# Performance work log

Hardware: AMD Instinct MI355X
Metric: run time of the kernel (lower is better)

## Reference

```python
import jax, jax.numpy as jnp
import numpy as np

DIM = 256
NUM_HEADS = 8
HEAD_DIM = DIM // NUM_HEADS      # 32
KEY_DIM = HEAD_DIM // 2          # attn_ratio=0.5 -> 16
SCALE = KEY_DIM ** -0.5
H_QKV = DIM + 2 * KEY_DIM * NUM_HEADS  # 512
EPS = 1e-5


def bn(y, gamma, beta, mean, var):
    # eval-mode BatchNorm2d over channel dim of NCHW
    inv = jax.lax.rsqrt(var + EPS) * gamma
    return y * inv[None, :, None, None] + (beta - mean * inv)[None, :, None, None]


def setup_inputs() -> dict:
    key = jax.random.key(0)
    ks = jax.random.split(key, 16)
    B, C, H, W = 16, DIM, 32, 32
    x = jax.random.normal(ks[0], (B, C, H, W), dtype=jnp.float32)
    w_qkv = jax.random.normal(ks[1], (H_QKV, C), dtype=jnp.float32) * 0.05
    g_qkv = jax.random.uniform(ks[2], (H_QKV,), minval=0.5, maxval=1.5)
    b_qkv = jax.random.normal(ks[3], (H_QKV,)) * 0.1
    m_qkv = jax.random.normal(ks[4], (H_QKV,)) * 0.1
    v_qkv = jax.random.uniform(ks[5], (H_QKV,), minval=0.5, maxval=1.5)
    w_pos = jax.random.normal(ks[6], (C, 1, 3, 3), dtype=jnp.float32) * 0.1
    g_pos = jax.random.uniform(ks[7], (C,), minval=0.5, maxval=1.5)
    b_pos = jax.random.normal(ks[8], (C,)) * 0.1
    m_pos = jax.random.normal(ks[9], (C,)) * 0.1
    v_pos = jax.random.uniform(ks[10], (C,), minval=0.5, maxval=1.5)
    w_proj = jax.random.normal(ks[11], (C, C), dtype=jnp.float32) * 0.05
    g_proj = jax.random.uniform(ks[12], (C,), minval=0.5, maxval=1.5)
    b_proj = jax.random.normal(ks[13], (C,)) * 0.1
    m_proj = jax.random.normal(ks[14], (C,)) * 0.1
    v_proj = jax.random.uniform(ks[15], (C,), minval=0.5, maxval=1.5)
    return dict(x=x, w_qkv=w_qkv, g_qkv=g_qkv, b_qkv=b_qkv, m_qkv=m_qkv, v_qkv=v_qkv,
                w_pos=w_pos, g_pos=g_pos, b_pos=b_pos, m_pos=m_pos, v_pos=v_pos,
                w_proj=w_proj, g_proj=g_proj, b_proj=b_proj, m_proj=m_proj, v_proj=v_proj)


def reference(x, w_qkv, g_qkv, b_qkv, m_qkv, v_qkv,
              w_pos, g_pos, b_pos, m_pos, v_pos,
              w_proj, g_proj, b_proj, m_proj, v_proj):
    B, C, H, W = x.shape
    N = H * W
    # 1x1 conv (no bias) + BN
    qkv = bn(jnp.einsum('bchw,oc->bohw', x, w_qkv), g_qkv, b_qkv, m_qkv, v_qkv)
    qkv = qkv.reshape(B, NUM_HEADS, 2 * KEY_DIM + HEAD_DIM, N)
    q = qkv[:, :, :KEY_DIM]                 # [B, h, kd, N]
    k = qkv[:, :, KEY_DIM:2 * KEY_DIM]      # [B, h, kd, N]
    v = qkv[:, :, 2 * KEY_DIM:]             # [B, h, hd, N]
    # attention: q^T k, softmax over keys
    scores = jnp.einsum('bhkn,bhkm->bhnm', q, k) * SCALE  # [B, h, N, N]
    attn = jax.nn.softmax(scores, axis=-1)
    # v @ attn^T -> [B, h, hd, N]
    attended = jnp.einsum('bhdn,bhmn->bhdm', v, attn).reshape(B, C, H, W)
    # depthwise 3x3 positional encoding on v + BN, residual add
    v_img = v.reshape(B, C, H, W)
    pos = jax.lax.conv_general_dilated(
        v_img, w_pos, window_strides=(1, 1), padding=((1, 1), (1, 1)),
        dimension_numbers=('NCHW', 'OIHW', 'NCHW'), feature_group_count=C)
    pos = bn(pos, g_pos, b_pos, m_pos, v_pos)
    out = attended + pos
    # final 1x1 projection + BN
    out = bn(jnp.einsum('bchw,oc->bohw', out, w_proj), g_proj, b_proj, m_proj, v_proj)
    return out
```

## Files before the change

### kernel.cpp

```cpp
#include <hip/hip_runtime.h>

typedef short v8s __attribute__((ext_vector_type(8)));
typedef float v4f __attribute__((ext_vector_type(4)));
typedef unsigned short u16;

#define NPIX 1024
#define EPS 1e-5f

__device__ __forceinline__ float bf2f(u16 u){
  return __uint_as_float(((unsigned)u) << 16);
}
__device__ __forceinline__ u16 f2bf(float f){
  unsigned b = __float_as_uint(f);
  b += 0x7FFF + ((b >> 16) & 1);
  return (u16)(b >> 16);
}
__device__ __forceinline__ unsigned cvtpk(float lo, float hi){
  unsigned r;
  asm("v_cvt_pk_bf16_f32 %0, %1, %2" : "=v"(r) : "v"(lo), "v"(hi));
  return r;
}
__device__ __forceinline__ float exp2n(float x){
#if __has_builtin(__builtin_amdgcn_exp2f)
  return __builtin_amdgcn_exp2f(x);
#else
  float r; asm("v_exp_f32 %0, %1" : "=v"(r) : "v"(x)); return r;
#endif
}

template<bool OUT_F32>
__global__ __launch_bounds__(256) void gemm_bn(
    const float* __restrict__ src, const float* __restrict__ W,
    const float* __restrict__ gam, const float* __restrict__ bet,
    const float* __restrict__ mu,  const float* __restrict__ var,
    u16* __restrict__ bout, float* __restrict__ fout, int Cin, int Cout)
{
  const int n0 = blockIdx.x * 64;
  const int o0 = blockIdx.y * 64;
  const int b  = blockIdx.z;
  const int tid = threadIdx.x;
  const int w = tid >> 6, lane = tid & 63, col = lane & 15, quad = lane >> 4;

  __shared__ u16 Wl[2][64 * 40];
  __shared__ u16 Sr[2][64 * 40];

  const int o = o0 + w * 16 + col;
  const float inv = rsqrtf(var[o] + EPS) * gam[o];
  const float add = bet[o] - mu[o] * inv;

  v4f acc[4];
#pragma unroll
  for (int i = 0; i < 4; i++) acc[i] = (v4f){0.f, 0.f, 0.f, 0.f};

  const int so = tid >> 2, sks = (tid & 3) * 8;
  const int sp = tid & 63, skg = (tid >> 6) * 8;

  const float* wp = W + (size_t)(o0 + so) * Cin + sks;
  const float* sb = src + (size_t)b * Cin * NPIX + n0 + sp;

  float4 wa = ((const float4*)wp)[0];
  float4 wb = ((const float4*)wp)[1];
  float sv[8];
#pragma unroll
  for (int i = 0; i < 8; i++) sv[i] = sb[(size_t)(skg + i) * NPIX];

  const int nt = Cin >> 5;
  int cur = 0;
  for (int t = 0; t < nt; ++t) {
    {
      uint4 pk;
      pk.x = cvtpk(wa.x, wa.y);
      pk.y = cvtpk(wa.z, wa.w);
      pk.z = cvtpk(wb.x, wb.y);
      pk.w = cvtpk(wb.z, wb.w);
      *(uint4*)(&Wl[cur][so * 40 + sks]) = pk;
    }
    {
      uint4 pk;
      pk.x = cvtpk(sv[0], sv[1]);
      pk.y = cvtpk(sv[2], sv[3]);
      pk.z = cvtpk(sv[4], sv[5]);
      pk.w = cvtpk(sv[6], sv[7]);
      *(uint4*)(&Sr[cur][sp * 40 + skg]) = pk;
    }
    if (t + 1 < nt) {
      const float* wpn = wp + (t + 1) * 32;
      wa = ((const float4*)wpn)[0];
      wb = ((const float4*)wpn)[1];
      const float* sbn = sb + (size_t)((t + 1) * 32 + skg) * NPIX;
#pragma unroll
      for (int i = 0; i < 8; i++) sv[i] = sbn[(size_t)i * NPIX];
    }
    __syncthreads();

    v8s bfrag = *(const v8s*)(&Wl[cur][(w * 16 + col) * 40 + quad * 8]);
#pragma unroll
    for (int mt = 0; mt < 4; mt++) {
      v8s af = *(const v8s*)(&Sr[cur][(mt * 16 + col) * 40 + quad * 8]);
      acc[mt] = __builtin_amdgcn_mfma_f32_16x16x32_bf16(af, bfrag, acc[mt], 0, 0, 0);
    }
    cur ^= 1;
  }

  const size_t orow = (size_t)(b * Cout + o) * NPIX + n0 + quad * 4;
#pragma unroll
  for (int mt = 0; mt < 4; mt++) {
    float v0 = acc[mt][0] * inv + add;
    float v1 = acc[mt][1] * inv + add;
    float v2 = acc[mt][2] * inv + add;
    float v3 = acc[mt][3] * inv + add;
    if (OUT_F32) {
      *(float4*)(&fout[orow + mt * 16]) = make_float4(v0, v1, v2, v3);
    } else {
      uint2 pk;
      pk.x = cvtpk(v0, v1);
      pk.y = cvtpk(v2, v3);
      *(uint2*)(&bout[orow + mt * 16]) = pk;
    }
  }
}

__global__ __launch_bounds__(256) void attn_mfma_kernel(
    const u16* __restrict__ qkv, float* __restrict__ att,
    const float* __restrict__ wpos,
    const float* __restrict__ g_pos, const float* __restrict__ b_pos,
    const float* __restrict__ m_pos, const float* __restrict__ v_pos)
{
  const int qt = blockIdx.x, h = blockIdx.y, b = blockIdx.z;
  const int tid = threadIdx.x, w = tid >> 6, lane = tid & 63;
  const int col = lane & 15, quad = lane >> 4;
  const u16* base = qkv + (size_t)(b * 512 + h * 64) * NPIX;

  __shared__ u16 Kt[2][64 * 24];
  __shared__ u16 Vl[2][32 * 72];
  __shared__ u16 Pl[4][16 * 72];

  const int q0 = qt * 64 + w * 16;

  v8s qf = (v8s){0, 0, 0, 0, 0, 0, 0, 0};
  if (quad < 2) {
#pragma unroll
    for (int jj = 0; jj < 8; jj++) {
      int k = quad * 8 + jj;
      qf[jj] = (short)f2bf(bf2f(base[(size_t)k * NPIX + q0 + col])
                           * 0.36067376022224085f);
    }
  }

  float lsum = 0.f;
  v4f o_acc[2];
  o_acc[0] = (v4f){0, 0, 0, 0};
  o_acc[1] = (v4f){0, 0, 0, 0};

  const int kk4 = w * 4;
  const int vd = tid >> 3, vjs = (tid & 7) * 8;

  ushort4 kr;
  kr.x = base[(size_t)(16 + kk4 + 0) * NPIX + lane];
  kr.y = base[(size_t)(16 + kk4 + 1) * NPIX + lane];
  kr.z = base[(size_t)(16 + kk4 + 2) * NPIX + lane];
  kr.w = base[(size_t)(16 + kk4 + 3) * NPIX + lane];
  uint4 vr = *(const uint4*)(base + (size_t)(32 + vd) * NPIX + vjs);

  int cur = 0;
  for (int t = 0; t < 16; ++t) {
    *(ushort4*)(&Kt[cur][lane * 24 + kk4]) = kr;
    *(uint4*)(&Vl[cur][vd * 72 + vjs]) = vr;
    if (t < 15) {
      const int j0n = (t + 1) * 64;
      kr.x = base[(size_t)(16 + kk4 + 0) * NPIX + j0n + lane];
      kr.y = base[(size_t)(16 + kk4 + 1) * NPIX + j0n + lane];
      kr.z = base[(size_t)(16 + kk4 + 2) * NPIX + j0n + lane];
      kr.w = base[(size_t)(16 + kk4 + 3) * NPIX + j0n + lane];
      vr = *(const uint4*)(base + (size_t)(32 + vd) * NPIX + j0n + vjs);
    }
    __syncthreads();

#pragma unroll
    for (int jt = 0; jt < 4; jt++) {
      v8s kf = (v8s){0, 0, 0, 0, 0, 0, 0, 0};
      if (quad < 2)
        kf = *(const v8s*)(&Kt[cur][(jt * 16 + col) * 24 + quad * 8]);
      v4f z = (v4f){0, 0, 0, 0};
      v4f s = __builtin_amdgcn_mfma_f32_16x16x32_bf16(kf, qf, z, 0, 0, 0);
      float p0 = exp2n(s[0]);
      float p1 = exp2n(s[1]);
      float p2 = exp2n(s[2]);
      float p3 = exp2n(s[3]);
      lsum += (p0 + p1) + (p2 + p3);
      uint2 pk;
      pk.x = cvtpk(p0, p1);
      pk.y = cvtpk(p2, p3);
      *(uint2*)(&Pl[w][col * 72 + jt * 16 + quad * 4]) = pk;
    }

#pragma unroll
    for (int T = 0; T < 2; T++) {
      v8s pf = *(const v8s*)(&Pl[w][col * 72 + T * 32 + quad * 8]);
#pragma unroll
      for (int dt = 0; dt < 2; dt++) {
        v8s vf = *(const v8s*)(&Vl[cur][(dt * 16 + col) * 72 + T * 32 + quad * 8]);
        o_acc[dt] = __builtin_amdgcn_mfma_f32_16x16x32_bf16(pf, vf, o_acc[dt], 0, 0, 0);
      }
    }
    cur ^= 1;
  }

  lsum += __shfl_xor(lsum, 16);
  lsum += __shfl_xor(lsum, 32);
  float ls[4];
#pragma unroll
  for (int r = 0; r < 4; r++) ls[r] = __shfl(lsum, quad * 4 + r);

  const int p0 = q0 + quad * 4;
  const int y  = p0 >> 5, x0 = p0 & 31;

#pragma unroll
  for (int dt = 0; dt < 2; dt++) {
    const int cl = dt * 16 + col;
    const int ca = h * 32 + cl;
    const u16* vrow = base + (size_t)(32 + cl) * NPIX;
    const float* w9 = wpos + ca * 9;
    const float cinv = rsqrtf(v_pos[ca] + EPS) * g_pos[ca];
    const float cadd = b_pos[ca] - m_pos[ca] * cinv;

    float cv0 = 0.f, cv1 = 0.f, cv2 = 0.f, cv3 = 0.f;
#pragma unroll
    for (int ky = 0; ky < 3; ky++) {
      const int yy = y + ky - 1;
      if (yy < 0 || yy > 31) continue;
      const u16* rp = vrow + yy * 32 + x0;
      const float w0 = w9[ky * 3 + 0];
      const float w1 = w9[ky * 3 + 1];
      const float w2 = w9[ky * 3 + 2];
      const float tm = (x0 >= 1)      ? bf2f(rp[-1]) : 0.f;
      const float t0 = bf2f(rp[0]);
      const float t1 = bf2f(rp[1]);
      const float t2 = bf2f(rp[2]);
      const float t3 = bf2f(rp[3]);
      const float t4 = (x0 + 4 <= 31) ? bf2f(rp[4]) : 0.f;
      cv0 += tm * w0 + t0 * w1 + t1 * w2;
      cv1 += t0 * w0 + t1 * w1 + t2 * w2;
      cv2 += t1 * w0 + t2 * w1 + t3 * w2;
      cv3 += t2 * w0 + t3 * w1 + t4 * w2;
    }

    float4 pack;
    pack.x = o_acc[dt][0] * (1.f / ls[0]) + cv0 * cinv + cadd;
    pack.y = o_acc[dt][1] * (1.f / ls[1]) + cv1 * cinv + cadd;
    pack.z = o_acc[dt][2] * (1.f / ls[2]) + cv2 * cinv + cadd;
    pack.w = o_acc[dt][3] * (1.f / ls[3]) + cv3 * cinv + cadd;
    *(float4*)(&att[(size_t)(b * 256 + ca) * NPIX + p0]) = pack;
  }
}

extern "C" void kernel_launch(void* const* d_in, const int* in_sizes, int n_in,
                              void* d_out, int out_size, void* d_ws, size_t ws_size,
                              hipStream_t stream)
{
  (void)in_sizes; (void)n_in; (void)out_size; (void)ws_size;
  const float* x      = (const float*)d_in[0];
  const float* w_qkv  = (const float*)d_in[1];
  const float* g_qkv  = (const float*)d_in[2];
  const float* b_qkv  = (const float*)d_in[3];
  const float* m_qkv  = (const float*)d_in[4];
  const float* v_qkv  = (const float*)d_in[5];
  const float* w_pos  = (const float*)d_in[6];
  const float* g_pos  = (const float*)d_in[7];
  const float* b_pos  = (const float*)d_in[8];
  const float* m_pos  = (const float*)d_in[9];
  const float* v_pos  = (const float*)d_in[10];
  const float* w_proj = (const float*)d_in[11];
  const float* g_proj = (const float*)d_in[12];
  const float* b_proj = (const float*)d_in[13];
  const float* m_proj = (const float*)d_in[14];
  const float* v_proj = (const float*)d_in[15];

  u16*   qkv = (u16*)d_ws;
  float* att = (float*)d_in[0];

  gemm_bn<false><<<dim3(16, 8, 16), 256, 0, stream>>>(
      x, w_qkv, g_qkv, b_qkv, m_qkv, v_qkv, qkv, nullptr, 256, 512);
  attn_mfma_kernel<<<dim3(16, 8, 16), 256, 0, stream>>>(
      qkv, att, w_pos, g_pos, b_pos, m_pos, v_pos);
  gemm_bn<true><<<dim3(16, 4, 16), 256, 0, stream>>>(
      att, w_proj, g_proj, b_proj, m_proj, v_proj, nullptr,
      (float*)d_out, 256, 256);
}
```

Measured before the change: 160.4 us.

## Use 128-deep K tiles in GEMM and swizzle attention LDS layouts

The GEMM now stages 128 input channels per phase in a single LDS buffer instead of double-buffered 32-channel tiles with register prefetch, so there are fewer barriers per K but global loads no longer overlap compute. The attention kernel widens the K tile stride to 40 and zero-fills it once, which removes the per-lane conditional on K fragment loads. It also applies an XOR-style slot rotation to V rows in LDS to cut bank conflicts. Losing the prefetch overlap in the GEMM risks exposing load latency.

Result: slower. 177.0 us (+10.4%).

```diff
diff --git a/kernel.cpp b/kernel.cpp
--- a/kernel.cpp
+++ b/kernel.cpp
@@ -41,8 +41,8 @@
   const int tid = threadIdx.x;
   const int w = tid >> 6, lane = tid & 63, col = lane & 15, quad = lane >> 4;
 
-  __shared__ u16 Wl[2][64 * 40];
-  __shared__ u16 Sr[2][64 * 40];
+  __shared__ u16 Wl[64 * 136];
+  __shared__ u16 Sr[64 * 136];
 
   const int o = o0 + w * 16 + col;
   const float inv = rsqrtf(var[o] + EPS) * gam[o];
@@ -52,54 +52,55 @@
 #pragma unroll
   for (int i = 0; i < 4; i++) acc[i] = (v4f){0.f, 0.f, 0.f, 0.f};
 
-  const int so = tid >> 2, sks = (tid & 3) * 8;
-  const int sp = tid & 63, skg = (tid >> 6) * 8;
+  const int so = tid >> 2, sks = (tid & 3) * 32;
+  const int sp = tid & 63, skg = (tid >> 6) * 32;
 
   const float* wp = W + (size_t)(o0 + so) * Cin + sks;
   const float* sb = src + (size_t)b * Cin * NPIX + n0 + sp;
 
-  float4 wa = ((const float4*)wp)[0];
-  float4 wb = ((const float4*)wp)[1];
-  float sv[8];
-#pragma unroll
-  for (int i = 0; i < 8; i++) sv[i] = sb[(size_t)(skg + i) * NPIX];
-
-  const int nt = Cin >> 5;
-  int cur = 0;
-  for (int t = 0; t < nt; ++t) {
+  const int nph = Cin >> 7;
+  for (int ph = 0; ph < nph; ++ph) {
+    if (ph) __syncthreads();
     {
-      uint4 pk;
-      pk.x = cvtpk(wa.x, wa.y);
-      pk.y = cvtpk(wa.z, wa.w);
-      pk.z = cvtpk(wb.x, wb.y);
-      pk.w = cvtpk(wb.z, wb.w);
-      *(uint4*)(&Wl[cur][so * 40 + sks]) = pk;
+      const float* p = wp + ph * 128;
+#pragma unroll
+      for (int tch = 0; tch < 4; ++tch) {
+        float4 f0 = ((const float4*)p)[tch * 2];
+        float4 f1 = ((const float4*)p)[tch * 2 + 1];
+        uint4 pk;
+        pk.x = cvtpk(f0.x, f0.y);
+        pk.y = cvtpk(f0.z, f0.w);
+        pk.z = cvtpk(f1.x, f1.y);
+        pk.w = cvtpk(f1.z, f1.w);
+        *(uint4*)(&Wl[so * 136 + sks + tch * 8]) = pk;
+      }
     }
     {
-      uint4 pk;
-      pk.x = cvtpk(sv[0], sv[1]);
-      pk.y = cvtpk(sv[2], sv[3]);
-      pk.z = cvtpk(sv[4], sv[5]);
-      pk.w = cvtpk(sv[6], sv[7]);
-      *(uint4*)(&Sr[cur][sp * 40 + skg]) = pk;
-    }
-    if (t + 1 < nt) {
-      const float* wpn = wp + (t + 1) * 32;
-      wa = ((const float4*)wpn)[0];
-      wb = ((const float4*)wpn)[1];
-      const float* sbn = sb + (size_t)((t + 1) * 32 + skg) * NPIX;
-#pragma unroll
-      for (int i = 0; i < 8; i++) sv[i] = sbn[(size_t)i * NPIX];
+      const float* p = sb + (size_t)(ph * 128 + skg) * NPIX;
+#pragma unroll
+      for (int tch = 0; tch < 4; ++tch) {
+        float f[8];
+#pragma unroll
+        for (int i = 0; i < 8; ++i) f[i] = p[(size_t)(tch * 8 + i) * NPIX];
+        uint4 pk;
+        pk.x = cvtpk(f[0], f[1]);
+        pk.y = cvtpk(f[2], f[3]);
+        pk.z = cvtpk(f[4], f[5]);
+        pk.w = cvtpk(f[6], f[7]);
+        *(uint4*)(&Sr[sp * 136 + skg + tch * 8]) = pk;
+      }
     }
     __syncthreads();
 
-    v8s bfrag = *(const v8s*)(&Wl[cur][(w * 16 + col) * 40 + quad * 8]);
-#pragma unroll
-    for (int mt = 0; mt < 4; mt++) {
-      v8s af = *(const v8s*)(&Sr[cur][(mt * 16 + col) * 40 + quad * 8]);
-      acc[mt] = __builtin_amdgcn_mfma_f32_16x16x32_bf16(af, bfrag, acc[mt], 0, 0, 0);
-    }
-    cur ^= 1;
+#pragma unroll
+    for (int ks = 0; ks < 4; ++ks) {
+      v8s bfrag = *(const v8s*)(&Wl[(w * 16 + col) * 136 + ks * 32 + quad * 8]);
+#pragma unroll
+      for (int mt = 0; mt < 4; mt++) {
+        v8s af = *(const v8s*)(&Sr[(mt * 16 + col) * 136 + ks * 32 + quad * 8]);
+        acc[mt] = __builtin_amdgcn_mfma_f32_16x16x32_bf16(af, bfrag, acc[mt], 0, 0, 0);
+      }
+    }
   }
 
   const size_t orow = (size_t)(b * Cout + o) * NPIX + n0 + quad * 4;
@@ -131,9 +132,16 @@
   const int col = lane & 15, quad = lane >> 4;
   const u16* base = qkv + (size_t)(b * 512 + h * 64) * NPIX;
 
-  __shared__ u16 Kt[2][64 * 24];
+  __shared__ u16 Kt[2][64 * 40];
   __shared__ u16 Vl[2][32 * 72];
   __shared__ u16 Pl[4][16 * 72];
+
+  {
+    uint4 z = make_uint4(0, 0, 0, 0);
+    uint4* kflat = (uint4*)&Kt[0][0];
+    for (int i = tid; i < 640; i += 256) kflat[i] = z;
+  }
+  __syncthreads();
 
   const int q0 = qt * 64 + w * 16;
 
@@ -154,6 +162,10 @@
 
   const int kk4 = w * 4;
   const int vd = tid >> 3, vjs = (tid & 7) * 8;
+  const int vslot = ((tid & 7) + vd) & 7;
+
+  const int vs0 = (quad + (col & 7)) & 7;
+  const int vs1 = vs0 ^ 4;
 
   ushort4 kr;
   kr.x = base[(size_t)(16 + kk4 + 0) * NPIX + lane];
@@ -164,8 +176,8 @@
 
   int cur = 0;
   for (int t = 0; t < 16; ++t) {
-    *(ushort4*)(&Kt[cur][lane * 24 + kk4]) = kr;
-    *(uint4*)(&Vl[cur][vd * 72 + vjs]) = vr;
+    *(ushort4*)(&Kt[cur][lane * 40 + kk4]) = kr;
+    *(uint4*)(&Vl[cur][vd * 72 + vslot * 8]) = vr;
     if (t < 15) {
       const int j0n = (t + 1) * 64;
       kr.x = base[(size_t)(16 + kk4 + 0) * NPIX + j0n + lane];
@@ -178,9 +190,7 @@
 
 #pragma unroll
     for (int jt = 0; jt < 4; jt++) {
-      v8s kf = (v8s){0, 0, 0, 0, 0, 0, 0, 0};
-      if (quad < 2)
-        kf = *(const v8s*)(&Kt[cur][(jt * 16 + col) * 24 + quad * 8]);
+      v8s kf = *(const v8s*)(&Kt[cur][(jt * 16 + col) * 40 + quad * 8]);
       v4f z = (v4f){0, 0, 0, 0};
       v4f s = __builtin_amdgcn_mfma_f32_16x16x32_bf16(kf, qf, z, 0, 0, 0);
       float p0 = exp2n(s[0]);
@@ -197,9 +207,10 @@
 #pragma unroll
     for (int T = 0; T < 2; T++) {
       v8s pf = *(const v8s*)(&Pl[w][col * 72 + T * 32 + quad * 8]);
+      const int vs = T ? vs1 : vs0;
 #pragma unroll
       for (int dt = 0; dt < 2; dt++) {
-        v8s vf = *(const v8s*)(&Vl[cur][(dt * 16 + col) * 72 + T * 32 + quad * 8]);
+        v8s vf = *(const v8s*)(&Vl[cur][(dt * 16 + col) * 72 + vs * 8]);
         o_acc[dt] = __builtin_amdgcn_mfma_f32_16x16x32_bf16(pf, vf, o_acc[dt], 0, 0, 0);
       }
     }
```

## Store attention output as transposed bf16 for direct projection GEMM loads

Applied to the files above, without the earlier changes.

The attention kernel now writes its output in bf16 with a pixel-major, channel-minor layout instead of fp32 NCHW. The projection GEMM gets a BSRC mode that loads eight contiguous bf16 channels with one vector load and stores them to shared memory without conversion. This halves intermediate traffic and replaces eight strided scalar loads per thread with one. The cost is that the attention epilogue now does four scattered 2-byte stores, 512 bytes apart, per thread, which may coalesce poorly.

New measurement: 163.7 us. +2.1%, slower.

```diff
diff --git a/kernel.cpp b/kernel.cpp
--- a/kernel.cpp
+++ b/kernel.cpp
@@ -28,9 +28,9 @@
 #endif
 }
 
-template<bool OUT_F32>
+template<bool OUT_F32, bool BSRC>
 __global__ __launch_bounds__(256) void gemm_bn(
-    const float* __restrict__ src, const float* __restrict__ W,
+    const void* __restrict__ srcv, const float* __restrict__ W,
     const float* __restrict__ gam, const float* __restrict__ bet,
     const float* __restrict__ mu,  const float* __restrict__ var,
     u16* __restrict__ bout, float* __restrict__ fout, int Cin, int Cout)
@@ -41,6 +41,9 @@
   const int tid = threadIdx.x;
   const int w = tid >> 6, lane = tid & 63, col = lane & 15, quad = lane >> 4;
 
+  const float* srcf = (const float*)srcv;
+  const u16*   srcb = (const u16*)srcv;
+
   __shared__ u16 Wl[2][64 * 40];
   __shared__ u16 Sr[2][64 * 40];
 
@@ -56,13 +59,18 @@
   const int sp = tid & 63, skg = (tid >> 6) * 8;
 
   const float* wp = W + (size_t)(o0 + so) * Cin + sks;
-  const float* sb = src + (size_t)b * Cin * NPIX + n0 + sp;
 
   float4 wa = ((const float4*)wp)[0];
   float4 wb = ((const float4*)wp)[1];
   float sv[8];
-#pragma unroll
-  for (int i = 0; i < 8; i++) sv[i] = sb[(size_t)(skg + i) * NPIX];
+  v8s svb;
+  if (BSRC) {
+    svb = *(const v8s*)(&srcb[((size_t)b * NPIX + n0 + sp) * Cin + skg]);
+  } else {
+    const float* sb = srcf + ((size_t)b * Cin) * NPIX + n0 + sp;
+#pragma unroll
+    for (int i = 0; i < 8; i++) sv[i] = sb[(size_t)(skg + i) * NPIX];
+  }
 
   const int nt = Cin >> 5;
   int cur = 0;
@@ -75,7 +83,9 @@
       pk.w = cvtpk(wb.z, wb.w);
       *(uint4*)(&Wl[cur][so * 40 + sks]) = pk;
     }
-    {
+    if (BSRC) {
+      *(v8s*)(&Sr[cur][sp * 40 + skg]) = svb;
+    } else {
       uint4 pk;
       pk.x = cvtpk(sv[0], sv[1]);
       pk.y = cvtpk(sv[2], sv[3]);
@@ -87,9 +97,15 @@
       const float* wpn = wp + (t + 1) * 32;
       wa = ((const float4*)wpn)[0];
       wb = ((const float4*)wpn)[1];
-      const float* sbn = sb + (size_t)((t + 1) * 32 + skg) * NPIX;
-#pragma unroll
-      for (int i = 0; i < 8; i++) sv[i] = sbn[(size_t)i * NPIX];
+      if (BSRC) {
+        svb = *(const v8s*)(&srcb[((size_t)b * NPIX + n0 + sp) * Cin +
+                                  (t + 1) * 32 + skg]);
+      } else {
+        const float* sbn = srcf + ((size_t)b * Cin) * NPIX + n0 + sp +
+                           (size_t)((t + 1) * 32 + skg) * NPIX;
+#pragma unroll
+        for (int i = 0; i < 8; i++) sv[i] = sbn[(size_t)i * NPIX];
+      }
     }
     __syncthreads();
 
@@ -121,7 +137,7 @@
 }
 
 __global__ __launch_bounds__(256) void attn_mfma_kernel(
-    const u16* __restrict__ qkv, float* __restrict__ att,
+    const u16* __restrict__ qkv, u16* __restrict__ attT,
     const float* __restrict__ wpos,
     const float* __restrict__ g_pos, const float* __restrict__ b_pos,
     const float* __restrict__ m_pos, const float* __restrict__ v_pos)
@@ -245,12 +261,18 @@
       cv3 += t2 * w0 + t3 * w1 + t4 * w2;
     }
 
-    float4 pack;
-    pack.x = o_acc[dt][0] * (1.f / ls[0]) + cv0 * cinv + cadd;
-    pack.y = o_acc[dt][1] * (1.f / ls[1]) + cv1 * cinv + cadd;
-    pack.z = o_acc[dt][2] * (1.f / ls[2]) + cv2 * cinv + cadd;
-    pack.w = o_acc[dt][3] * (1.f / ls[3]) + cv3 * cinv + cadd;
-    *(float4*)(&att[(size_t)(b * 256 + ca) * NPIX + p0]) = pack;
+    const float o0v = o_acc[dt][0] * (1.f / ls[0]) + cv0 * cinv + cadd;
+    const float o1v = o_acc[dt][1] * (1.f / ls[1]) + cv1 * cinv + cadd;
+    const float o2v = o_acc[dt][2] * (1.f / ls[2]) + cv2 * cinv + cadd;
+    const float o3v = o_acc[dt][3] * (1.f / ls[3]) + cv3 * cinv + cadd;
+
+    const unsigned pa = cvtpk(o0v, o1v);
+    const unsigned pb = cvtpk(o2v, o3v);
+    const size_t ab = ((size_t)b * NPIX + p0) * 256 + ca;
+    attT[ab          ] = (u16)pa;
+    attT[ab + 256    ] = (u16)(pa >> 16);
+    attT[ab + 512    ] = (u16)pb;
+    attT[ab + 768    ] = (u16)(pb >> 16);
   }
 }
 
@@ -276,14 +298,14 @@
   const float* m_proj = (const float*)d_in[14];
   const float* v_proj = (const float*)d_in[15];
 
-  u16*   qkv = (u16*)d_ws;
-  float* att = (float*)d_in[0];
-
-  gemm_bn<false><<<dim3(16, 8, 16), 256, 0, stream>>>(
+  u16* qkv  = (u16*)d_ws;
+  u16* attT = (u16*)d_in[0];
+
+  gemm_bn<false, false><<<dim3(16, 8, 16), 256, 0, stream>>>(
       x, w_qkv, g_qkv, b_qkv, m_qkv, v_qkv, qkv, nullptr, 256, 512);
   attn_mfma_kernel<<<dim3(16, 8, 16), 256, 0, stream>>>(
-      qkv, att, w_pos, g_pos, b_pos, m_pos, v_pos);
-  gemm_bn<true><<<dim3(16, 4, 16), 256, 0, stream>>>(
-      att, w_proj, g_proj, b_proj, m_proj, v_proj, nullptr,
+      qkv, attT, w_pos, g_pos, b_pos, m_pos, v_pos);
+  gemm_bn<true, true><<<dim3(16, 4, 16), 256, 0, stream>>>(
+      attT, w_proj, g_proj, b_proj, m_proj, v_proj, nullptr,
       (float*)d_out, 256, 256);
 }
```
